# Kernel optimization log

Measured on AMD Instinct MI355X. Metric: run time of the kernel, lower is better.

Reference implementation:

```python
import jax, jax.numpy as jnp
import numpy as np

NUM_HEADS = 12
HEAD_DIM = 64
DIM = NUM_HEADS * HEAD_DIM  # 768
WIN = 14
REL = 2 * WIN - 1  # 27


def setup_inputs() -> dict:
    key = jax.random.key(0)
    ks = jax.random.split(key, 7)
    B, N = 256, WIN * WIN
    return {
        "x": jax.random.normal(ks[0], (B, N, DIM), dtype=jnp.float32),
        "qkv_w": jax.random.normal(ks[1], (3 * DIM, DIM), dtype=jnp.float32) * 0.02,
        "qkv_b": jnp.zeros((3 * DIM,), dtype=jnp.float32),
        "rel_pos_h": jax.random.normal(ks[2], (REL, HEAD_DIM), dtype=jnp.float32) * 0.02,
        "rel_pos_w": jax.random.normal(ks[3], (REL, HEAD_DIM), dtype=jnp.float32) * 0.02,
        "proj_w": jax.random.normal(ks[4], (DIM, DIM), dtype=jnp.float32) * 0.02,
        "proj_b": jnp.zeros((DIM,), dtype=jnp.float32),
        "H": WIN,
        "W": WIN,
    }


def _rel_pos_bias(q, rel_pos_h, rel_pos_w, H, W):
    # q: [B, heads, H*W, d] (already scaled). q_shape == k_shape == (H, W), ratios == 1.
    dist_h = jnp.arange(H)[:, None] - jnp.arange(H)[None, :] + (H - 1)  # [H, H]
    dist_w = jnp.arange(W)[:, None] - jnp.arange(W)[None, :] + (W - 1)  # [W, W]
    Rh = rel_pos_h[dist_h]  # [H, H, d]
    Rw = rel_pos_w[dist_w]  # [W, W, d]
    B, nh = q.shape[0], q.shape[1]
    r_q = q.reshape(B, nh, H, W, q.shape[-1])
    rel_h = jnp.einsum("bnhwd,hkd->bnhwk", r_q, Rh)  # [B, nh, H, W, Hk]
    rel_w = jnp.einsum("bnhwd,wkd->bnhwk", r_q, Rw)  # [B, nh, H, W, Wk]
    return rel_h[..., :, None] + rel_w[..., None, :]  # [B, nh, H, W, Hk, Wk]


def reference(x, qkv_w, qkv_b, rel_pos_h, rel_pos_w, proj_w, proj_b, H, W):
    B, N, C = x.shape
    d = C // NUM_HEADS
    scale = d ** -0.5
    qkv = x @ qkv_w.T + qkv_b  # [B, N, 3C]
    qkv = qkv.reshape(B, N, 3, NUM_HEADS, d).transpose(2, 0, 3, 1, 4)
    q, k, v = qkv[0], qkv[1], qkv[2]  # [B, nh, N, d]
    q = q * scale
    attn = jnp.einsum("bhqd,bhkd->bhqk", q, k)  # [B, nh, N, N]
    bias = _rel_pos_bias(q, rel_pos_h, rel_pos_w, H, W)
    attn = (attn.reshape(B, NUM_HEADS, H, W, H, W) + bias).reshape(B, NUM_HEADS, N, N)
    attn = jax.nn.softmax(attn, axis=-1)
    out = jnp.einsum("bhqk,bhkd->bhqd", attn, v)  # [B, nh, N, d]
    out = out.transpose(0, 2, 1, 3).reshape(B, N, C)
    return out @ proj_w.T + proj_b
```

## Files before the change

### kernel.cpp

```cpp
#include <hip/hip_runtime.h>
#include <stdint.h>


typedef __attribute__((ext_vector_type(8))) short bf16x8;
typedef __attribute__((ext_vector_type(4))) float f32x4;
typedef __attribute__((ext_vector_type(4))) unsigned int u32x4;
typedef unsigned short u16;
typedef unsigned int u32;

__device__ __forceinline__ u16 f2bf(float f) {
  u32 x = __float_as_uint(f);
  x += 0x7fffu + ((x >> 16) & 1u);
  return (u16)(x >> 16);
}

__device__ __forceinline__ u32 pack2bf(float a, float b) {
  return (u32)f2bf(a) | ((u32)f2bf(b) << 16);
}

__device__ __forceinline__ void gload_lds16(const void* g, void* l) {
  __builtin_amdgcn_global_load_lds(
      (__attribute__((address_space(1))) void*)g,
      (__attribute__((address_space(3))) void*)l, 16, 0, 0);
}

__global__ __launch_bounds__(256) void cvt_bf16(const float* __restrict__ src,
                                                u16* __restrict__ dst, int n4) {
  int i = blockIdx.x * 256 + threadIdx.x;
  if (i < n4) {
    float4 f = ((const float4*)src)[i];
    uint2 p;
    p.x = pack2bf(f.x, f.y);
    p.y = pack2bf(f.z, f.w);
    ((uint2*)dst)[i] = p;
  }
}

__device__ __forceinline__ void stage8(const u16* pA, const u16* pB,
                                       char* dstA, int k0) {
#pragma unroll
  for (int i = 0; i < 4; i++)
    gload_lds16(pA + (size_t)i * 49152 + k0, dstA + i * 8192);
#pragma unroll
  for (int i = 0; i < 4; i++)
    gload_lds16(pB + (size_t)i * 49152 + k0, dstA + 32768 + i * 8192);
}

template <int MODE, int NT>
__global__ __launch_bounds__(512, 2) void gemm256(
    const u16* __restrict__ A, const u16* __restrict__ W,
    const float* __restrict__ bias, u16* __restrict__ qb, u16* __restrict__ kb,
    u16* __restrict__ vb, float* __restrict__ outf) {
  __shared__ char lds[131072];

  const int t = threadIdx.x;
  const int lane = t & 63, wv = t >> 6;
  const int quad = lane >> 4, l15 = lane & 15;
  const int wm = wv >> 2, wn = wv & 3;

  const u32 nwg = gridDim.x;
  const u32 wg = blockIdx.x;
  const u32 qd = nwg >> 3, rm = nwg & 7;
  const u32 xcd = wg & 7, loc = wg >> 3;
  const u32 swz = (xcd < rm) ? (xcd * (qd + 1) + loc)
                             : (rm * (qd + 1) + (xcd - rm) * qd + loc);
  const int mtile = swz / NT;
  const int ntile = (int)swz - mtile * NT;
  const int m0 = mtile << 8, n0 = ntile << 8;

  const int srow = t >> 3;
  const int scol = ((t & 7) ^ (srow & 7)) << 3;
  const u16* pA = A + (size_t)(m0 + srow) * 768 + scol;
  const u16* pB = W + (size_t)(n0 + srow) * 768 + scol;
  char* sdst = lds + t * 16;

  const int swz0 = ((quad) ^ (l15 & 7)) << 4;
  const int swz1 = ((4 + quad) ^ (l15 & 7)) << 4;
  const int arow = (wm * 128 + l15) * 128;
  const int brow = 32768 + (wn * 64 + l15) * 128;

  f32x4 acc[8][4];
#pragma unroll
  for (int i = 0; i < 8; i++)
#pragma unroll
    for (int j = 0; j < 4; j++) acc[i][j] = (f32x4){0.f, 0.f, 0.f, 0.f};

  stage8(pA, pB, sdst, 0);
  asm volatile("s_waitcnt vmcnt(0)" ::: "memory");
  __builtin_amdgcn_s_barrier();

  bf16x8 af[4][2], bfr[4][2];
  for (int kt = 0; kt < 12; ++kt) {
    char* bufc = lds + ((kt & 1) << 16);
    char* nsdst = sdst + (((kt & 1) ^ 1) << 16);
    const int k0n = (kt + 1) << 6;

#pragma unroll
    for (int mf = 0; mf < 4; mf++) {
      af[mf][0] = *(const bf16x8*)(bufc + arow + mf * 2048 + swz0);
      af[mf][1] = *(const bf16x8*)(bufc + arow + mf * 2048 + swz1);
    }
#pragma unroll
    for (int nf = 0; nf < 2; nf++) {
      bfr[nf][0] = *(const bf16x8*)(bufc + brow + nf * 2048 + swz0);
      bfr[nf][1] = *(const bf16x8*)(bufc + brow + nf * 2048 + swz1);
    }
    if (kt < 11) stage8(pA, pB, nsdst, k0n);
    __builtin_amdgcn_s_barrier();
    asm volatile("s_waitcnt lgkmcnt(0)" ::: "memory");
    __builtin_amdgcn_s_setprio(1);
#pragma unroll
    for (int k = 0; k < 2; k++)
#pragma unroll
      for (int mf = 0; mf < 4; mf++)
#pragma unroll
        for (int nf = 0; nf < 2; nf++)
          acc[mf][nf] = __builtin_amdgcn_mfma_f32_16x16x32_bf16(
              af[mf][k], bfr[nf][k], acc[mf][nf], 0, 0, 0);
    __builtin_amdgcn_s_setprio(0);
    __builtin_amdgcn_s_barrier();

#pragma unroll
    for (int nf = 2; nf < 4; nf++) {
      bfr[nf][0] = *(const bf16x8*)(bufc + brow + nf * 2048 + swz0);
      bfr[nf][1] = *(const bf16x8*)(bufc + brow + nf * 2048 + swz1);
    }
    __builtin_amdgcn_s_barrier();
    asm volatile("s_waitcnt lgkmcnt(0)" ::: "memory");
    __builtin_amdgcn_s_setprio(1);
#pragma unroll
    for (int k = 0; k < 2; k++)
#pragma unroll
      for (int mf = 0; mf < 4; mf++)
#pragma unroll
        for (int nf = 2; nf < 4; nf++)
          acc[mf][nf] = __builtin_amdgcn_mfma_f32_16x16x32_bf16(
              af[mf][k], bfr[nf][k], acc[mf][nf], 0, 0, 0);
    __builtin_amdgcn_s_setprio(0);
    __builtin_amdgcn_s_barrier();

#pragma unroll
    for (int mf = 0; mf < 4; mf++) {
      af[mf][0] = *(const bf16x8*)(bufc + arow + (mf + 4) * 2048 + swz0);
      af[mf][1] = *(const bf16x8*)(bufc + arow + (mf + 4) * 2048 + swz1);
    }
    __builtin_amdgcn_s_barrier();
    asm volatile("s_waitcnt lgkmcnt(0)" ::: "memory");
    __builtin_amdgcn_s_setprio(1);
#pragma unroll
    for (int k = 0; k < 2; k++)
#pragma unroll
      for (int mf = 0; mf < 4; mf++)
#pragma unroll
        for (int nf = 0; nf < 2; nf++)
          acc[mf + 4][nf] = __builtin_amdgcn_mfma_f32_16x16x32_bf16(
              af[mf][k], bfr[nf][k], acc[mf + 4][nf], 0, 0, 0);
    __builtin_amdgcn_s_setprio(0);
    __builtin_amdgcn_s_barrier();

    __builtin_amdgcn_s_setprio(1);
#pragma unroll
    for (int k = 0; k < 2; k++)
#pragma unroll
      for (int mf = 0; mf < 4; mf++)
#pragma unroll
        for (int nf = 2; nf < 4; nf++)
          acc[mf + 4][nf] = __builtin_amdgcn_mfma_f32_16x16x32_bf16(
              af[mf][k], bfr[nf][k], acc[mf + 4][nf], 0, 0, 0);
    __builtin_amdgcn_s_setprio(0);
    asm volatile("s_waitcnt vmcnt(0)" ::: "memory");
    __builtin_amdgcn_s_barrier();
  }

  if (MODE == 0) {
    const int which = n0 / 768;
    u16* dst = (which == 0) ? qb : ((which == 1) ? kb : vb);
    const float sc = (which == 0) ? 0.125f : 1.0f;
    float bs[4];
    size_t hb[4];
#pragma unroll
    for (int nf = 0; nf < 4; nf++) {
      int n = n0 + wn * 64 + nf * 16 + l15;
      int cc = n - which * 768;
      bs[nf] = bias[n];
      hb[nf] = (size_t)(cc >> 6) * 12544 + (size_t)(cc & 63);
    }
#pragma unroll
    for (int mf = 0; mf < 8; mf++) {
#pragma unroll
      for (int r = 0; r < 4; r++) {
        int m = m0 + wm * 128 + mf * 16 + (quad << 2) + r;
        int bb = m / 196;
        int tok = m - bb * 196;
        size_t rb = (size_t)bb * 150528 + (size_t)tok * 64;
#pragma unroll
        for (int nf = 0; nf < 4; nf++)
          dst[rb + hb[nf]] = f2bf((acc[mf][nf][r] + bs[nf]) * sc);
      }
    }
  } else {
    float bs[4];
#pragma unroll
    for (int nf = 0; nf < 4; nf++)
      bs[nf] = bias[n0 + wn * 64 + nf * 16 + l15];
#pragma unroll
    for (int mf = 0; mf < 8; mf++) {
#pragma unroll
      for (int r = 0; r < 4; r++) {
        int m = m0 + wm * 128 + mf * 16 + (quad << 2) + r;
#pragma unroll
        for (int nf = 0; nf < 4; nf++)
          outf[(size_t)m * 768 + (n0 + wn * 64 + nf * 16 + l15)] =
              acc[mf][nf][r] + bs[nf];
      }
    }
  }
}

__global__ __launch_bounds__(256) void attn_fused(
    const u16* __restrict__ qbuf, const u16* __restrict__ kbuf,
    const u16* __restrict__ vbuf, const float* __restrict__ rel_h,
    const float* __restrict__ rel_w, u16* __restrict__ aout) {
  __shared__ u16 Vt[26 * 512];
  __shared__ float TL[4][2][28][16];

  const int t = threadIdx.x;
  const int bh = blockIdx.x;
  const int b = bh / 12, h = bh - b * 12;
  const int lane = t & 63, wv = t >> 6;
  const int quad = lane >> 4, l15 = lane & 15;
  const size_t base = (size_t)bh * (196 * 64);

  for (int c = t; c < 196 * 8; c += 256) {
    int row = c >> 3, seg = c & 7;
    uint4 vv = *(const uint4*)(vbuf + base + row * 64 + seg * 8);
    const u16* pv8 = (const u16*)&vv;
    u16* dst = Vt + (row >> 3) * 512 + (row & 7);
#pragma unroll
    for (int e = 0; e < 8; e++) {
      int ee = (e + seg) & 7;
      dst[(seg * 8 + ee) * 8] = pv8[ee];
    }
  }
  for (int i = t; i < 12 * 64; i += 256) {
    int k = 196 + (i >> 6), d = i & 63;
    Vt[(k >> 3) * 512 + d * 8 + (k & 7)] = 0;
  }

  bf16x8 brl[2][2][2];
#pragma unroll
  for (int half = 0; half < 2; half++) {
    const float* relp = half ? rel_w : rel_h;
#pragma unroll
    for (int nt = 0; nt < 2; nt++) {
      int ridx = nt * 16 + l15;
      if (ridx > 26) ridx = 26;
#pragma unroll
      for (int ks = 0; ks < 2; ks++) {
        const float* p = relp + ridx * 64 + ks * 32 + quad * 8;
        float4 f0 = *(const float4*)p;
        float4 f1 = *(const float4*)(p + 4);
        bf16x8 r;
        r[0] = (short)f2bf(f0.x); r[1] = (short)f2bf(f0.y);
        r[2] = (short)f2bf(f0.z); r[3] = (short)f2bf(f0.w);
        r[4] = (short)f2bf(f1.x); r[5] = (short)f2bf(f1.y);
        r[6] = (short)f2bf(f1.z); r[7] = (short)f2bf(f1.w);
        brl[half][nt][ks] = r;
      }
    }
  }
  __syncthreads();

  float (*TLh)[16] = TL[wv][0];
  float (*TLw)[16] = TL[wv][1];
  const u16* kB = kbuf + base;
  const u16* qB = qbuf + base;

  for (int qt = wv; qt < 13; qt += 4) {
    int qrl = qt * 16 + l15;
    if (qrl > 195) qrl = 195;
    bf16x8 aq0 = *(const bf16x8*)(qB + qrl * 64 + quad * 8);
    bf16x8 aq1 = *(const bf16x8*)(qB + qrl * 64 + 32 + quad * 8);
    const int hq = qrl / 14, wq = qrl - hq * 14;

#pragma unroll
    for (int half = 0; half < 2; half++) {
#pragma unroll
      for (int nt = 0; nt < 2; nt++) {
        f32x4 tc = (f32x4){0.f, 0.f, 0.f, 0.f};
        tc = __builtin_amdgcn_mfma_f32_16x16x32_bf16(brl[half][nt][0], aq0, tc, 0, 0, 0);
        tc = __builtin_amdgcn_mfma_f32_16x16x32_bf16(brl[half][nt][1], aq1, tc, 0, 0, 0);
#pragma unroll
        for (int r = 0; r < 4; r++) {
          int r27 = nt * 16 + quad * 4 + r;
          if (r27 < 27) TL[wv][half][r27][l15] = tc[r];
        }
      }
    }

    f32x4 oacc[4];
#pragma unroll
    for (int dt = 0; dt < 4; dt++) oacc[dt] = (f32x4){0.f, 0.f, 0.f, 0.f};
    float sm = 0.f;
    const int srcA = l15 + ((quad & 1) << 5);
    const bool hi = (quad >> 1) != 0;

#pragma unroll 2
    for (int st = 0; st < 6; st++) {
      u32 pw[2][2];
#pragma unroll
      for (int u = 0; u < 2; u++) {
        const int kt = st * 2 + u;
        const int keyl = kt * 16 + l15;
        bf16x8 bk0 = *(const bf16x8*)(kB + keyl * 64 + quad * 8);
        bf16x8 bk1 = *(const bf16x8*)(kB + keyl * 64 + 32 + quad * 8);
        f32x4 s = (f32x4){0.f, 0.f, 0.f, 0.f};
        s = __builtin_amdgcn_mfma_f32_16x16x32_bf16(bk0, aq0, s, 0, 0, 0);
        s = __builtin_amdgcn_mfma_f32_16x16x32_bf16(bk1, aq1, s, 0, 0, 0);
        const int key0 = kt * 16 + quad * 4;
        const int hk0 = key0 / 14, wk0 = key0 - 14 * hk0;
        float pr[4];
#pragma unroll
        for (int r = 0; r < 4; r++) {
          int cr = (wk0 + r >= 14) ? 1 : 0;
          int hk = hk0 + cr, wk = wk0 + r - 14 * cr;
          float v = s[r] + TLh[hq - hk + 13][l15] + TLw[wq - wk + 13][l15];
          float p = __expf(v);
          pr[r] = p;
          sm += p;
        }
        pw[u][0] = pack2bf(pr[0], pr[1]);
        pw[u][1] = pack2bf(pr[2], pr[3]);
      }
      u32 a0 = __shfl(pw[0][0], srcA),      b0 = __shfl(pw[1][0], srcA);
      u32 a1 = __shfl(pw[0][1], srcA),      b1 = __shfl(pw[1][1], srcA);
      u32 a2 = __shfl(pw[0][0], srcA + 16), b2 = __shfl(pw[1][0], srcA + 16);
      u32 a3 = __shfl(pw[0][1], srcA + 16), b3 = __shfl(pw[1][1], srcA + 16);
      u32x4 pbw = (u32x4){hi ? b0 : a0, hi ? b1 : a1, hi ? b2 : a2, hi ? b3 : a3};
      bf16x8 pb = __builtin_bit_cast(bf16x8, pbw);
#pragma unroll
      for (int dt = 0; dt < 4; dt++) {
        bf16x8 av = *(const bf16x8*)(Vt + (st * 4 + quad) * 512 + (dt * 16 + l15) * 8);
        oacc[dt] = __builtin_amdgcn_mfma_f32_16x16x32_bf16(av, pb, oacc[dt], 0, 0, 0);
      }
    }

    {
      const int keyl = 192 + l15;
      const int keyc = (keyl > 195) ? 195 : keyl;
      bf16x8 bk0 = *(const bf16x8*)(kB + keyc * 64 + quad * 8);
      bf16x8 bk1 = *(const bf16x8*)(kB + keyc * 64 + 32 + quad * 8);
      f32x4 s = (f32x4){0.f, 0.f, 0.f, 0.f};
      s = __builtin_amdgcn_mfma_f32_16x16x32_bf16(bk0, aq0, s, 0, 0, 0);
      s = __builtin_amdgcn_mfma_f32_16x16x32_bf16(bk1, aq1, s, 0, 0, 0);
      const int key0 = 192 + quad * 4;
      const int hk0 = key0 / 14, wk0 = key0 - 14 * hk0;
      const bool valid = (quad == 0);
      float pr[4];
#pragma unroll
      for (int r = 0; r < 4; r++) {
        int cr = (wk0 + r >= 14) ? 1 : 0;
        int hk = hk0 + cr, wk = wk0 + r - 14 * cr;
        int ih = hq - hk + 13; ih = ih < 0 ? 0 : ih;
        int iw = wq - wk + 13; iw = iw < 0 ? 0 : iw;
        float v = s[r] + TLh[ih][l15] + TLw[iw][l15];
        float p = valid ? __expf(v) : 0.f;
        pr[r] = p;
        sm += p;
      }
      u32 pw0 = pack2bf(pr[0], pr[1]);
      u32 pw1 = pack2bf(pr[2], pr[3]);
      const int srcA = l15 + ((quad & 1) << 5);
      const bool hi = (quad >> 1) != 0;
      u32 a0 = __shfl(pw0, srcA);
      u32 a1 = __shfl(pw1, srcA);
      u32 a2 = __shfl(pw0, srcA + 16);
      u32 a3 = __shfl(pw1, srcA + 16);
      u32x4 pbw = (u32x4){hi ? 0u : a0, hi ? 0u : a1, hi ? 0u : a2, hi ? 0u : a3};
      bf16x8 pb = __builtin_bit_cast(bf16x8, pbw);
#pragma unroll
      for (int dt = 0; dt < 4; dt++) {
        bf16x8 av = (bf16x8){0, 0, 0, 0, 0, 0, 0, 0};
        if (quad < 2)
          av = *(const bf16x8*)(Vt + (24 + quad) * 512 + (dt * 16 + l15) * 8);
        oacc[dt] = __builtin_amdgcn_mfma_f32_16x16x32_bf16(av, pb, oacc[dt], 0, 0, 0);
      }
    }

    sm += __shfl_xor(sm, 16, 64);
    sm += __shfl_xor(sm, 32, 64);
    const float inv = 1.0f / sm;

    const int qrow = qt * 16 + l15;
    if (qrow < 196) {
      u16* op = aout + ((size_t)(b * 196 + qrow) * 12 + h) * 64;
#pragma unroll
      for (int dt = 0; dt < 4; dt++) {
        uint2 stv;
        stv.x = pack2bf(oacc[dt][0] * inv, oacc[dt][1] * inv);
        stv.y = pack2bf(oacc[dt][2] * inv, oacc[dt][3] * inv);
        *(uint2*)(op + dt * 16 + quad * 4) = stv;
      }
    }
  }
}

extern "C" void kernel_launch(void* const* d_in, const int* in_sizes, int n_in,
                              void* d_out, int out_size, void* d_ws, size_t ws_size,
                              hipStream_t stream) {
  (void)in_sizes; (void)n_in; (void)out_size; (void)ws_size;
  const float* x      = (const float*)d_in[0];
  const float* qkv_w  = (const float*)d_in[1];
  const float* qkv_b  = (const float*)d_in[2];
  const float* rel_h  = (const float*)d_in[3];
  const float* rel_w  = (const float*)d_in[4];
  const float* proj_w = (const float*)d_in[5];
  const float* proj_b = (const float*)d_in[6];
  float* out = (float*)d_out;

  char* ws = (char*)d_ws;
  u16* xbf  = (u16*)(ws);
  u16* qbuf = (u16*)(ws + 77070336);
  u16* kbuf = (u16*)(ws + 154140672);
  u16* vbuf = (u16*)(ws + 231211008);
  u16* wqb  = (u16*)(ws + 308281344);
  u16* wpb  = (u16*)(ws + 311820288);

  cvt_bf16<<<37632, 256, 0, stream>>>(x, xbf, 38535168 / 4);
  cvt_bf16<<<1728, 256, 0, stream>>>(qkv_w, wqb, 1769472 / 4);
  cvt_bf16<<<576, 256, 0, stream>>>(proj_w, wpb, 589824 / 4);

  gemm256<0, 9><<<1764, 512, 0, stream>>>(xbf, wqb, qkv_b, qbuf, kbuf, vbuf,
                                          nullptr);
  attn_fused<<<3072, 256, 0, stream>>>(qbuf, kbuf, vbuf, rel_h, rel_w, xbf);
  gemm256<1, 3><<<588, 512, 0, stream>>>(xbf, wpb, proj_b, nullptr, nullptr,
                                         nullptr, out);
}
```

Before: 846.3 us.

## Process two query tiles per wave to reuse K and V fragments

Each wave now handles a pair of 16-row query tiles. Every loaded K fragment and V fragment feeds MFMAs for both tiles, which halves the per-query global/LDS load traffic and raises instruction-level parallelism. The relative-position tables are resized per wave (the height table is windowed by the pair's starting row and padded to 33 columns) to hold both tiles. The cost is higher register pressure and uneven work across the four waves (7 pairs over 4 waves).

```diff
diff --git a/kernel.cpp b/kernel.cpp
--- a/kernel.cpp
+++ b/kernel.cpp
@@ -222,7 +222,8 @@
     const u16* __restrict__ vbuf, const float* __restrict__ rel_h,
     const float* __restrict__ rel_w, u16* __restrict__ aout) {
   __shared__ u16 Vt[26 * 512];
-  __shared__ float TL[4][2][28][16];
+  __shared__ float TLh[4][17][33];
+  __shared__ float TLw[4][28][33];
 
   const int t = threadIdx.x;
   const int bh = blockIdx.x;
@@ -271,77 +272,104 @@
   }
   __syncthreads();
 
-  float (*TLh)[16] = TL[wv][0];
-  float (*TLw)[16] = TL[wv][1];
   const u16* kB = kbuf + base;
   const u16* qB = qbuf + base;
 
-  for (int qt = wv; qt < 13; qt += 4) {
-    int qrl = qt * 16 + l15;
-    if (qrl > 195) qrl = 195;
-    bf16x8 aq0 = *(const bf16x8*)(qB + qrl * 64 + quad * 8);
-    bf16x8 aq1 = *(const bf16x8*)(qB + qrl * 64 + 32 + quad * 8);
-    const int hq = qrl / 14, wq = qrl - hq * 14;
-
-#pragma unroll
-    for (int half = 0; half < 2; half++) {
-#pragma unroll
-      for (int nt = 0; nt < 2; nt++) {
-        f32x4 tc = (f32x4){0.f, 0.f, 0.f, 0.f};
-        tc = __builtin_amdgcn_mfma_f32_16x16x32_bf16(brl[half][nt][0], aq0, tc, 0, 0, 0);
-        tc = __builtin_amdgcn_mfma_f32_16x16x32_bf16(brl[half][nt][1], aq1, tc, 0, 0, 0);
-#pragma unroll
-        for (int r = 0; r < 4; r++) {
-          int r27 = nt * 16 + quad * 4 + r;
-          if (r27 < 27) TL[wv][half][r27][l15] = tc[r];
+  for (int p = wv; p < 7; p += 4) {
+    const int qt0 = 2 * p;
+    const int h0 = (32 * p) / 14;
+
+    bf16x8 aq0[2], aq1[2];
+    int hqv[2], wqv[2], hbv[2];
+#pragma unroll
+    for (int j = 0; j < 2; j++) {
+      int qrl = (qt0 + j) * 16 + l15;
+      if (qrl > 195) qrl = 195;
+      aq0[j] = *(const bf16x8*)(qB + qrl * 64 + quad * 8);
+      aq1[j] = *(const bf16x8*)(qB + qrl * 64 + 32 + quad * 8);
+      hqv[j] = qrl / 14;
+      wqv[j] = qrl - hqv[j] * 14;
+      hbv[j] = hqv[j] + 13 - h0;
+    }
+
+#pragma unroll
+    for (int j = 0; j < 2; j++) {
+#pragma unroll
+      for (int half = 0; half < 2; half++) {
+#pragma unroll
+        for (int nt = 0; nt < 2; nt++) {
+          f32x4 tc = (f32x4){0.f, 0.f, 0.f, 0.f};
+          tc = __builtin_amdgcn_mfma_f32_16x16x32_bf16(brl[half][nt][0], aq0[j], tc, 0, 0, 0);
+          tc = __builtin_amdgcn_mfma_f32_16x16x32_bf16(brl[half][nt][1], aq1[j], tc, 0, 0, 0);
+#pragma unroll
+          for (int r = 0; r < 4; r++) {
+            int r27 = nt * 16 + quad * 4 + r;
+            if (half == 0) {
+              u32 ihh = (u32)(r27 - h0);
+              if (ihh < 17u) TLh[wv][ihh][l15 + 16 * j] = tc[r];
+            } else {
+              if (r27 < 27) TLw[wv][r27][l15 + 16 * j] = tc[r];
+            }
+          }
         }
       }
     }
 
-    f32x4 oacc[4];
-#pragma unroll
-    for (int dt = 0; dt < 4; dt++) oacc[dt] = (f32x4){0.f, 0.f, 0.f, 0.f};
-    float sm = 0.f;
+    f32x4 oacc[2][4];
+#pragma unroll
+    for (int j = 0; j < 2; j++)
+#pragma unroll
+      for (int dt = 0; dt < 4; dt++) oacc[j][dt] = (f32x4){0.f, 0.f, 0.f, 0.f};
+    float sm[2] = {0.f, 0.f};
     const int srcA = l15 + ((quad & 1) << 5);
     const bool hi = (quad >> 1) != 0;
 
-#pragma unroll 2
     for (int st = 0; st < 6; st++) {
-      u32 pw[2][2];
+      u32 pw[2][2][2];
 #pragma unroll
       for (int u = 0; u < 2; u++) {
         const int kt = st * 2 + u;
         const int keyl = kt * 16 + l15;
         bf16x8 bk0 = *(const bf16x8*)(kB + keyl * 64 + quad * 8);
         bf16x8 bk1 = *(const bf16x8*)(kB + keyl * 64 + 32 + quad * 8);
-        f32x4 s = (f32x4){0.f, 0.f, 0.f, 0.f};
-        s = __builtin_amdgcn_mfma_f32_16x16x32_bf16(bk0, aq0, s, 0, 0, 0);
-        s = __builtin_amdgcn_mfma_f32_16x16x32_bf16(bk1, aq1, s, 0, 0, 0);
         const int key0 = kt * 16 + quad * 4;
         const int hk0 = key0 / 14, wk0 = key0 - 14 * hk0;
-        float pr[4];
-#pragma unroll
-        for (int r = 0; r < 4; r++) {
-          int cr = (wk0 + r >= 14) ? 1 : 0;
-          int hk = hk0 + cr, wk = wk0 + r - 14 * cr;
-          float v = s[r] + TLh[hq - hk + 13][l15] + TLw[wq - wk + 13][l15];
-          float p = __expf(v);
-          pr[r] = p;
-          sm += p;
+#pragma unroll
+        for (int j = 0; j < 2; j++) {
+          f32x4 s = (f32x4){0.f, 0.f, 0.f, 0.f};
+          s = __builtin_amdgcn_mfma_f32_16x16x32_bf16(bk0, aq0[j], s, 0, 0, 0);
+          s = __builtin_amdgcn_mfma_f32_16x16x32_bf16(bk1, aq1[j], s, 0, 0, 0);
+          float pr[4];
+#pragma unroll
+          for (int r = 0; r < 4; r++) {
+            int cr = (wk0 + r >= 14) ? 1 : 0;
+            int hk = hk0 + cr, wk = wk0 + r - 14 * cr;
+            float v = s[r] + TLh[wv][hbv[j] - hk][l15 + 16 * j] +
+                      TLw[wv][wqv[j] - wk + 13][l15 + 16 * j];
+            float pe = __expf(v);
+            pr[r] = pe;
+            sm[j] += pe;
+          }
+          pw[j][u][0] = pack2bf(pr[0], pr[1]);
+          pw[j][u][1] = pack2bf(pr[2], pr[3]);
         }
-        pw[u][0] = pack2bf(pr[0], pr[1]);
-        pw[u][1] = pack2bf(pr[2], pr[3]);
-      }
-      u32 a0 = __shfl(pw[0][0], srcA),      b0 = __shfl(pw[1][0], srcA);
-      u32 a1 = __shfl(pw[0][1], srcA),      b1 = __shfl(pw[1][1], srcA);
-      u32 a2 = __shfl(pw[0][0], srcA + 16), b2 = __shfl(pw[1][0], srcA + 16);
-      u32 a3 = __shfl(pw[0][1], srcA + 16), b3 = __shfl(pw[1][1], srcA + 16);
-      u32x4 pbw = (u32x4){hi ? b0 : a0, hi ? b1 : a1, hi ? b2 : a2, hi ? b3 : a3};
-      bf16x8 pb = __builtin_bit_cast(bf16x8, pbw);
+      }
+      bf16x8 pb[2];
+#pragma unroll
+      for (int j = 0; j < 2; j++) {
+        u32 a0 = __shfl(pw[j][0][0], srcA),      b0 = __shfl(pw[j][1][0], srcA);
+        u32 a1 = __shfl(pw[j][0][1], srcA),      b1 = __shfl(pw[j][1][1], srcA);
+        u32 a2 = __shfl(pw[j][0][0], srcA + 16), b2 = __shfl(pw[j][1][0], srcA + 16);
+        u32 a3 = __shfl(pw[j][0][1], srcA + 16), b3 = __shfl(pw[j][1][1], srcA + 16);
+        u32x4 pbw = (u32x4){hi ? b0 : a0, hi ? b1 : a1, hi ? b2 : a2, hi ? b3 : a3};
+        pb[j] = __builtin_bit_cast(bf16x8, pbw);
+      }
 #pragma unroll
       for (int dt = 0; dt < 4; dt++) {
         bf16x8 av = *(const bf16x8*)(Vt + (st * 4 + quad) * 512 + (dt * 16 + l15) * 8);
-        oacc[dt] = __builtin_amdgcn_mfma_f32_16x16x32_bf16(av, pb, oacc[dt], 0, 0, 0);
+#pragma unroll
+        for (int j = 0; j < 2; j++)
+          oacc[j][dt] = __builtin_amdgcn_mfma_f32_16x16x32_bf16(av, pb[j], oacc[j][dt], 0, 0, 0);
       }
     }
 
@@ -350,56 +378,67 @@
       const int keyc = (keyl > 195) ? 195 : keyl;
       bf16x8 bk0 = *(const bf16x8*)(kB + keyc * 64 + quad * 8);
       bf16x8 bk1 = *(const bf16x8*)(kB + keyc * 64 + 32 + quad * 8);
-      f32x4 s = (f32x4){0.f, 0.f, 0.f, 0.f};
-      s = __builtin_amdgcn_mfma_f32_16x16x32_bf16(bk0, aq0, s, 0, 0, 0);
-      s = __builtin_amdgcn_mfma_f32_16x16x32_bf16(bk1, aq1, s, 0, 0, 0);
       const int key0 = 192 + quad * 4;
       const int hk0 = key0 / 14, wk0 = key0 - 14 * hk0;
       const bool valid = (quad == 0);
-      float pr[4];
-#pragma unroll
-      for (int r = 0; r < 4; r++) {
-        int cr = (wk0 + r >= 14) ? 1 : 0;
-        int hk = hk0 + cr, wk = wk0 + r - 14 * cr;
-        int ih = hq - hk + 13; ih = ih < 0 ? 0 : ih;
-        int iw = wq - wk + 13; iw = iw < 0 ? 0 : iw;
-        float v = s[r] + TLh[ih][l15] + TLw[iw][l15];
-        float p = valid ? __expf(v) : 0.f;
-        pr[r] = p;
-        sm += p;
-      }
-      u32 pw0 = pack2bf(pr[0], pr[1]);
-      u32 pw1 = pack2bf(pr[2], pr[3]);
-      const int srcA = l15 + ((quad & 1) << 5);
-      const bool hi = (quad >> 1) != 0;
-      u32 a0 = __shfl(pw0, srcA);
-      u32 a1 = __shfl(pw1, srcA);
-      u32 a2 = __shfl(pw0, srcA + 16);
-      u32 a3 = __shfl(pw1, srcA + 16);
-      u32x4 pbw = (u32x4){hi ? 0u : a0, hi ? 0u : a1, hi ? 0u : a2, hi ? 0u : a3};
-      bf16x8 pb = __builtin_bit_cast(bf16x8, pbw);
+      u32 pwt[2][2];
+#pragma unroll
+      for (int j = 0; j < 2; j++) {
+        f32x4 s = (f32x4){0.f, 0.f, 0.f, 0.f};
+        s = __builtin_amdgcn_mfma_f32_16x16x32_bf16(bk0, aq0[j], s, 0, 0, 0);
+        s = __builtin_amdgcn_mfma_f32_16x16x32_bf16(bk1, aq1[j], s, 0, 0, 0);
+        float pr[4];
+#pragma unroll
+        for (int r = 0; r < 4; r++) {
+          int cr = (wk0 + r >= 14) ? 1 : 0;
+          int hk = hk0 + cr, wk = wk0 + r - 14 * cr;
+          int ih = hbv[j] - hk; ih = ih < 0 ? 0 : ih;
+          int iw = wqv[j] - wk + 13; iw = iw < 0 ? 0 : iw;
+          float v = s[r] + TLh[wv][ih][l15 + 16 * j] + TLw[wv][iw][l15 + 16 * j];
+          float pe = valid ? __expf(v) : 0.f;
+          pr[r] = pe;
+          sm[j] += pe;
+        }
+        pwt[j][0] = pack2bf(pr[0], pr[1]);
+        pwt[j][1] = pack2bf(pr[2], pr[3]);
+      }
+      bf16x8 pb[2];
+#pragma unroll
+      for (int j = 0; j < 2; j++) {
+        u32 a0 = __shfl(pwt[j][0], srcA);
+        u32 a1 = __shfl(pwt[j][1], srcA);
+        u32 a2 = __shfl(pwt[j][0], srcA + 16);
+        u32 a3 = __shfl(pwt[j][1], srcA + 16);
+        u32x4 pbw = (u32x4){hi ? 0u : a0, hi ? 0u : a1, hi ? 0u : a2, hi ? 0u : a3};
+        pb[j] = __builtin_bit_cast(bf16x8, pbw);
+      }
 #pragma unroll
       for (int dt = 0; dt < 4; dt++) {
         bf16x8 av = (bf16x8){0, 0, 0, 0, 0, 0, 0, 0};
         if (quad < 2)
           av = *(const bf16x8*)(Vt + (24 + quad) * 512 + (dt * 16 + l15) * 8);
-        oacc[dt] = __builtin_amdgcn_mfma_f32_16x16x32_bf16(av, pb, oacc[dt], 0, 0, 0);
-      }
-    }
-
-    sm += __shfl_xor(sm, 16, 64);
-    sm += __shfl_xor(sm, 32, 64);
-    const float inv = 1.0f / sm;
-
-    const int qrow = qt * 16 + l15;
-    if (qrow < 196) {
-      u16* op = aout + ((size_t)(b * 196 + qrow) * 12 + h) * 64;
-#pragma unroll
-      for (int dt = 0; dt < 4; dt++) {
-        uint2 stv;
-        stv.x = pack2bf(oacc[dt][0] * inv, oacc[dt][1] * inv);
-        stv.y = pack2bf(oacc[dt][2] * inv, oacc[dt][3] * inv);
-        *(uint2*)(op + dt * 16 + quad * 4) = stv;
+#pragma unroll
+        for (int j = 0; j < 2; j++)
+          oacc[j][dt] = __builtin_amdgcn_mfma_f32_16x16x32_bf16(av, pb[j], oacc[j][dt], 0, 0, 0);
+      }
+    }
+
+#pragma unroll
+    for (int j = 0; j < 2; j++) {
+      float smj = sm[j];
+      smj += __shfl_xor(smj, 16, 64);
+      smj += __shfl_xor(smj, 32, 64);
+      const float inv = 1.0f / smj;
+      const int qrow = (qt0 + j) * 16 + l15;
+      if (qrow < 196) {
+        u16* op = aout + ((size_t)(b * 196 + qrow) * 12 + h) * 64;
+#pragma unroll
+        for (int dt = 0; dt < 4; dt++) {
+          uint2 stv;
+          stv.x = pack2bf(oacc[j][dt][0] * inv, oacc[j][dt][1] * inv);
+          stv.y = pack2bf(oacc[j][dt][2] * inv, oacc[j][dt][3] * inv);
+          *(uint2*)(op + dt * 16 + quad * 4) = stv;
+        }
       }
     }
   }
```

New measurement: 798.8 us. 5.6% less time.
